# Performance work log

Measured on AMD Instinct MI355X. Metric: run time of the kernel, lower is better.

Reference implementation:

```python
import jax, jax.numpy as jnp
import numpy as np

B, HP, WP, EMB = 32, 56, 56, 256
HEADS, WX, WY = 8, 7, 7
WS = WX * WY

# relative position index table (constant int lookup, matches torch buffer)
_idx = np.indices((WX, WY)).transpose(1, 2, 0).reshape(WS, 2)
_REL = _idx[None, :, :] - _idx[:, None, :] + np.array([WX - 1, WY - 1])  # [49,49,2]

# shift masks (constants)
_m = WX * (WY // 2)
_row = np.zeros((WS, WS), np.float32)
_row[-_m:, :-_m] = -np.inf
_row[:-_m, -_m:] = -np.inf
# rearrange '(r w1) (c w2) -> (w1 r) (w2 c)' with w1=WX, w2=WY
_col = _row.reshape(WS // WX, WX, WS // WY, WY).transpose(1, 0, 3, 2).reshape(WS, WS)
ROW_MASK = jnp.asarray(_row)
COL_MASK = jnp.asarray(_col)


def setup_inputs() -> dict:
    key = jax.random.key(0)
    k1, k2, k3 = jax.random.split(key, 3)
    x = jax.random.normal(k1, (B, HP, WP, EMB), jnp.float32)
    w1 = jax.random.normal(k2, (EMB, 3 * EMB), jnp.float32) * 0.02
    b1 = jnp.zeros((3 * EMB,), jnp.float32)
    pos_emb = jax.random.normal(k3, (2 * WX - 1, 2 * WY - 1), jnp.float32)
    return {"x": x, "w1": w1, "b1": b1, "pos_emb": pos_emb}


def reference(x, w1, b1, pos_emb):
    Bn, H, W, E = x.shape
    e = E // HEADS
    hdim = float(E) / HEADS
    qkv = x @ w1 + b1                         # [B,H,W,3E]
    qkv = qkv.reshape(Bn, H, W, E, 3)         # (c k): c outer, k inner (interleaved QKV)
    # shifted: roll by (-WX)//2 = -4 for WX=7 (Python floor div, as in source)
    qkv = jnp.roll(qkv, ((-WX) // 2, (-WY) // 2), axis=(1, 2))
    Wh, Ww = H // WX, W // WY
    # split channel (e H): head index is INNER dim, as in source rearrange
    t = qkv.reshape(Bn, Wh, WX, Ww, WY, e, HEADS, 3)
    t = t.transpose(0, 6, 1, 3, 2, 4, 5, 7).reshape(Bn, HEADS, Wh, Ww, WS, e, 3)
    q, k, v = t[..., 0], t[..., 1], t[..., 2]
    attn = jnp.einsum('bhuvqe,bhuvke->bhuvqk', q, k) / jnp.sqrt(
        jnp.asarray(hdim, x.dtype))
    bias = pos_emb[_REL[:, :, 0], _REL[:, :, 1]]   # [49,49]
    attn = attn + bias
    # shift masks on last window row / last window column (corner gets both)
    attn = attn.at[:, :, -1, :, :, :].add(ROW_MASK)
    attn = attn.at[:, :, :, -1, :, :].add(COL_MASK)
    out = jnp.einsum('bhuvqk,bhuvke->bhuvqe', jax.nn.softmax(attn, axis=-1), v)
    # merge back: channel = e*HEADS + h
    out = out.reshape(Bn, HEADS, Wh, Ww, WX, WY, e)
    out = out.transpose(0, 2, 4, 3, 5, 6, 1).reshape(Bn, H, W, E)
    # reverse roll uses WX//2 = +3 (NOT the inverse of -4), faithful to source
    out = jnp.roll(out, (WX // 2, WY // 2), axis=(1, 2))
    return out
```

## Files before the change

kernel.cpp:

```cpp
#include <hip/hip_runtime.h>


typedef short bf16x8 __attribute__((ext_vector_type(8)));
typedef float f32x4 __attribute__((ext_vector_type(4)));
typedef unsigned short u16;
typedef u16 u16x8 __attribute__((ext_vector_type(8)));
typedef u16 u16x4 __attribute__((ext_vector_type(4)));

#define MFMA16(A, B, C) __builtin_amdgcn_mfma_f32_16x16x32_bf16((A), (B), (C), 0, 0, 0)

__device__ __forceinline__ u16 f2bf(float f) {
  union { float f; unsigned int u; } c; c.f = f;
  unsigned int uu = c.u;
  return (u16)((uu + 0x7fffu + ((uu >> 16) & 1u)) >> 16);
}

#define OFF_A   16384
#define OFF_POS 50176
#define SMEM_BYTES (50176 + 896)

__global__ void prep_w(const float* __restrict__ w1, const float* __restrict__ b1,
                       u16* __restrict__ wT, float* __restrict__ bp) {
  int g = blockIdx.x * 256 + threadIdx.x;
  float val = w1[g];
  int n = g % 768;
  int k = g / 768;
  int t = n % 3, c = n / 3;
  int np = (c & 7) * 96 + t * 32 + (c >> 3);
  wT[np * 256 + k] = f2bf(val);
  if (g < 768) {
    int t2 = g % 3, c2 = g / 3;
    bp[(c2 & 7) * 96 + t2 * 32 + (c2 >> 3)] = b1[g];
  }
}

__launch_bounds__(512, 4)
__global__ void swin_fused(const float* __restrict__ x, const u16* __restrict__ wT,
                           const float* __restrict__ bp, const float* __restrict__ pos,
                           float* __restrict__ out) {
  __shared__ __align__(16) char smem[SMEM_BYTES];
  const int tid  = threadIdx.x;
  const int wave = tid >> 6;
  const int lane = tid & 63;
  const int quad = lane >> 4;
  const int l16  = lane & 15;
  const int blk  = blockIdx.x;
  const int b = blk >> 6, u = (blk >> 3) & 7, v = blk & 7;

  float* sPos = (float*)(smem + OFF_POS);
  if (tid < 169) sPos[(tid / 13) * 16 + tid % 13] = pos[tid];

  {
    const int xbase = b * (56 * 56 * 256);
#pragma unroll
    for (int it = 0; it < 4; ++it) {
      int idx = tid + it * 512;
      int row = idx >> 5;
      int ck  = idx & 31;
      char* dst = smem + OFF_A + row * 512 + ((ck ^ (row & 7)) << 4);
      u16x8 val{};
      if (row < 49) {
        int i = row / 7, j = row % 7;
        int sh = u * 7 + i + 4; if (sh >= 56) sh -= 56;
        int sw = v * 7 + j + 4; if (sw >= 56) sw -= 56;
        const float4* src = (const float4*)(x + xbase + (sh * 56 + sw) * 256 + ck * 8);
        float4 f0 = src[0];
        float4 f1 = src[1];
        val.s0 = f2bf(f0.x); val.s1 = f2bf(f0.y); val.s2 = f2bf(f0.z); val.s3 = f2bf(f0.w);
        val.s4 = f2bf(f1.x); val.s5 = f2bf(f1.y); val.s6 = f2bf(f1.z); val.s7 = f2bf(f1.w);
      }
      *(u16x8*)dst = val;
    }
  }

  float bias[6];
#pragma unroll
  for (int i = 0; i < 6; ++i) bias[i] = bp[wave * 96 + i * 16 + l16];

  __syncthreads();

  const char* sA = smem + OFF_A;
  char* T = smem + wave * 2048;
  bf16x8 qf[4], kf[4], vf[2][2];

#pragma unroll
  for (int t = 0; t < 3; ++t) {
    f32x4 acc[4][2];
#pragma unroll
    for (int m = 0; m < 4; ++m) {
      acc[m][0] = (f32x4){0.f, 0.f, 0.f, 0.f};
      acc[m][1] = (f32x4){0.f, 0.f, 0.f, 0.f};
    }
    const u16* gB0 = wT + (wave * 96 + t * 32 + l16) * 256 + quad * 8;
    const u16* gB1 = gB0 + 16 * 256;
    bf16x8 b0 = *(const bf16x8*)gB0;
    bf16x8 b1 = *(const bf16x8*)gB1;
#pragma unroll
    for (int ks = 0; ks < 8; ++ks) {
      bf16x8 b0n, b1n;
      if (ks < 7) {
        b0n = *(const bf16x8*)(gB0 + (ks + 1) * 32);
        b1n = *(const bf16x8*)(gB1 + (ks + 1) * 32);
      }
#pragma unroll
      for (int m = 0; m < 4; ++m) {
        int row = m * 16 + l16;
        bf16x8 am = *(const bf16x8*)(sA + row * 512 + (((ks * 4 + quad) ^ (row & 7)) << 4));
        acc[m][0] = MFMA16(am, b0, acc[m][0]);
        acc[m][1] = MFMA16(am, b1, acc[m][1]);
      }
      if (ks < 7) { b0 = b0n; b1 = b1n; }
    }

    if (t < 2) {
#pragma unroll
      for (int hm = 0; hm < 2; ++hm) {
#pragma unroll
        for (int m2 = 0; m2 < 2; ++m2) {
          int m = hm * 2 + m2;
#pragma unroll
          for (int r = 0; r < 4; ++r) {
            int rb = m2 * 16 + quad * 4 + r;
            int sw = (rb >> 2) & 3;
            char* base = T + (rb ^ ((rb >> 2) & 1)) * 64;
            *(u16*)(base + ((((l16 >> 3) ^ sw) << 4) | ((l16 & 7) << 1)))
                = f2bf(acc[m][0][r] + bias[t * 2]);
            *(u16*)(base + (((((l16 >> 3) + 2) ^ sw) << 4) | ((l16 & 7) << 1)))
                = f2bf(acc[m][1][r] + bias[t * 2 + 1]);
          }
        }
        asm volatile("s_waitcnt lgkmcnt(0)" ::: "memory");
#pragma unroll
        for (int m2 = 0; m2 < 2; ++m2) {
          int m = hm * 2 + m2;
          int rb = m2 * 16 + l16;
          int sw = (rb >> 2) & 3;
          const bf16x8 fr2 = *(const bf16x8*)(T + (rb ^ ((rb >> 2) & 1)) * 64
                                                + ((quad ^ sw) << 4));
          if (t == 0) qf[m] = fr2; else kf[m] = fr2;
        }
        asm volatile("s_waitcnt lgkmcnt(0)" ::: "memory");
      }
    } else {
#pragma unroll
      for (int i = 0; i < 2; ++i) {
#pragma unroll
        for (int m = 0; m < 4; ++m) {
          int kc = m * 2 + (quad >> 1);
          int hb = (quad & 1) << 3;
          u16x4 w;
          w.x = f2bf(acc[m][i][0] + bias[4 + i]);
          w.y = f2bf(acc[m][i][1] + bias[4 + i]);
          w.z = f2bf(acc[m][i][2] + bias[4 + i]);
          w.w = f2bf(acc[m][i][3] + bias[4 + i]);
          *(u16x4*)(T + l16 * 128 + (((kc ^ (l16 & 7)) << 4) | hb)) = w;
        }
        asm volatile("s_waitcnt lgkmcnt(0)" ::: "memory");
#pragma unroll
        for (int ph = 0; ph < 2; ++ph)
          vf[ph][i] = *(const bf16x8*)(T + l16 * 128 + (((ph * 4 + quad) ^ (l16 & 7)) << 4));
        asm volatile("s_waitcnt lgkmcnt(0)" ::: "memory");
      }
    }
  }

  int ki[4], kj[4]; bool kok[4], kro[4], kco[4];
#pragma unroll
  for (int n = 0; n < 4; ++n) {
    int k = n * 16 + l16;
    ki[n] = k / 7; kj[n] = k % 7;
    kok[n] = (k < 49);
    kro[n] = (ki[n] >= 4);
    kco[n] = (kj[n] >= 4);
  }
  const bool rowm = (u == 7), colm = (v == 7);
  const float scale = 0.17677669529663687f;

  f32x4 o[4][2];
  {
    char* T2 = T;
#pragma unroll
    for (int m = 0; m < 4; ++m) {
      f32x4 s[4];
#pragma unroll
      for (int n = 0; n < 4; ++n)
        s[n] = MFMA16(qf[m], kf[n], ((f32x4){0.f, 0.f, 0.f, 0.f}));

      float inv[4];
#pragma unroll
      for (int r = 0; r < 4; ++r) {
        int q = m * 16 + quad * 4 + r;
        int qi = q / 7, qj = q % 7;
        bool qro = (qi >= 4), qco = (qj >= 4);
        int cm = 102 - qi * 16 - qj;
        float sum = 0.f;
#pragma unroll
        for (int n = 0; n < 4; ++n) {
          bool bad = (!kok[n]) || (rowm && (qro != kro[n])) || (colm && (qco != kco[n]));
          float sv = bad ? -1e30f
                         : fminf(s[n][r] * scale + sPos[ki[n] * 16 + kj[n] + cm], 30.f);
          float p = __expf(sv);
          s[n][r] = p;
          sum += p;
        }
        sum += __shfl_xor(sum, 1);
        sum += __shfl_xor(sum, 2);
        sum += __shfl_xor(sum, 4);
        sum += __shfl_xor(sum, 8);
        inv[r] = 1.f / sum;
      }

#pragma unroll
      for (int n = 0; n < 4; ++n)
#pragma unroll
        for (int r = 0; r < 4; ++r) {
          int row16 = quad * 4 + r;
          int ch = (2 * n + (l16 >> 3) + 2 * quad) & 7;
          *(u16*)(T2 + row16 * 128 + ((ch << 4) | ((l16 & 7) << 1))) = f2bf(s[n][r]);
        }
      asm volatile("s_waitcnt lgkmcnt(0)" ::: "memory");
      bf16x8 pa0 = *(const bf16x8*)(T2 + l16 * 128 + (((quad + 2 * (l16 >> 2)) & 7) << 4));
      bf16x8 pa1 = *(const bf16x8*)(T2 + l16 * 128 + (((4 + quad + 2 * (l16 >> 2)) & 7) << 4));
      asm volatile("s_waitcnt lgkmcnt(0)" ::: "memory");

      o[m][0] = MFMA16(pa0, vf[0][0], ((f32x4){0.f, 0.f, 0.f, 0.f}));
      o[m][0] = MFMA16(pa1, vf[1][0], o[m][0]);
      o[m][1] = MFMA16(pa0, vf[0][1], ((f32x4){0.f, 0.f, 0.f, 0.f}));
      o[m][1] = MFMA16(pa1, vf[1][1], o[m][1]);
#pragma unroll
      for (int i = 0; i < 2; ++i)
#pragma unroll
        for (int r = 0; r < 4; ++r) o[m][i][r] *= inv[r];
    }
  }

  __syncthreads();
  {
    float* oLds = (float*)smem;
    const int hh = wave;
#pragma unroll
    for (int m = 0; m < 4; ++m)
#pragma unroll
      for (int r = 0; r < 4; ++r) {
        int row = m * 16 + quad * 4 + r;
        if (row < 49) {
          int t4 = row >> 2;
          int fr = (t4 + (t4 >> 1)) & 7;
#pragma unroll
          for (int n = 0; n < 2; ++n) {
            int ci = n * 32 + l16 * 2 + (hh >> 2);
            int cs = ci ^ fr;
            oLds[row * 256 + cs * 4 + (hh & 3)] = o[m][n][r];
          }
        }
      }
  }
  __syncthreads();

  {
    const int obase = b * (56 * 56 * 256);
    for (int i2 = tid; i2 < 49 * 64; i2 += 512) {
      int row = i2 >> 6, ck = i2 & 63;
      int ii = row / 7, jj = row % 7;
      int dh = u * 7 + ii + 3; if (dh >= 56) dh -= 56;
      int dw = v * 7 + jj + 3; if (dw >= 56) dw -= 56;
      int t4 = row >> 2;
      int fr = (t4 + (t4 >> 1)) & 7;
      f32x4 val = *(const f32x4*)((const float*)smem + row * 256 + 4 * (ck ^ fr));
      *(f32x4*)(out + obase + (dh * 56 + dw) * 256 + ck * 4) = val;
    }
  }
}

extern "C" void kernel_launch(void* const* d_in, const int* in_sizes, int n_in,
                              void* d_out, int out_size, void* d_ws, size_t ws_size,
                              hipStream_t stream) {
  const float* x   = (const float*)d_in[0];
  const float* w1  = (const float*)d_in[1];
  const float* b1  = (const float*)d_in[2];
  const float* pos = (const float*)d_in[3];
  const size_t need = (size_t)768 * 256 * 2 + 768 * 4;
  if (ws_size < need) return;
  u16*   wT = (u16*)d_ws;
  float* bp = (float*)((char*)d_ws + 768 * 256 * 2);
  prep_w<<<768, 256, 0, stream>>>(w1, b1, wT, bp);
  swin_fused<<<2048, 512, 0, stream>>>(x, wT, bp, pos, (float*)d_out);
}
```

Measured before the change: 295.0 us.

## Compute transposed scores and pass P to PV MFMA via shuffles instead of LDS

The score MFMA swaps its operands so each lane holds one query row across keys. The row-sum reduction becomes two shuffles, and normalization moves before the bf16 pack. P is converted with v_cvt_pk_bf16_f32 and rearranged into the A-operand layout through cross-lane shuffles, replacing the LDS write/read round trip with its waitcnts. Key-side mask and position indices are precomputed as packed per-lane bitfields. Risks include more shuffle instructions and bf16 rounding of already-normalized probabilities.

```diff
diff --git a/kernel.cpp b/kernel.cpp
--- a/kernel.cpp
+++ b/kernel.cpp
@@ -13,6 +13,28 @@
   union { float f; unsigned int u; } c; c.f = f;
   unsigned int uu = c.u;
   return (u16)((uu + 0x7fffu + ((uu >> 16) & 1u)) >> 16);
+}
+
+__device__ __forceinline__ unsigned int cvtpk(float lo, float hi) {
+  unsigned int r;
+  asm("v_cvt_pk_bf16_f32 %0, %1, %2" : "=v"(r) : "v"(lo), "v"(hi));
+  return r;
+}
+
+__device__ __forceinline__ bf16x8 xchg(unsigned int p0a, unsigned int p1a,
+                                       unsigned int p0b, unsigned int p1b,
+                                       int quad, int l16) {
+  int lo = ((quad & 1) << 5) | l16;
+  int hi = lo + 16;
+  int a0 = __shfl((int)p0a, lo), b0 = __shfl((int)p0b, lo);
+  int a1 = __shfl((int)p1a, lo), b1 = __shfl((int)p1b, lo);
+  int a2 = __shfl((int)p0a, hi), b2 = __shfl((int)p0b, hi);
+  int a3 = __shfl((int)p1a, hi), b3 = __shfl((int)p1b, hi);
+  bool h = quad >= 2;
+  union { int u[4]; bf16x8 v; } r;
+  r.u[0] = h ? b0 : a0; r.u[1] = h ? b1 : a1;
+  r.u[2] = h ? b2 : a2; r.u[3] = h ? b3 : a3;
+  return r.v;
 }
 
 #define OFF_A   16384
@@ -164,74 +186,68 @@
     }
   }
 
-  int ki[4], kj[4]; bool kok[4], kro[4], kco[4];
+  unsigned int pb[4], fl[4];
 #pragma unroll
   for (int n = 0; n < 4; ++n) {
-    int k = n * 16 + l16;
-    ki[n] = k / 7; kj[n] = k % 7;
-    kok[n] = (k < 49);
-    kro[n] = (ki[n] >= 4);
-    kco[n] = (kj[n] >= 4);
+    pb[n] = 0; fl[n] = 0;
+#pragma unroll
+    for (int r = 0; r < 4; ++r) {
+      int k = n * 16 + quad * 4 + r;
+      int ki2 = k / 7, kj2 = k % 7;
+      bool kok = (k < 49);
+      pb[n] |= (unsigned int)(kok ? ki2 * 16 + kj2 : 0) << (8 * r);
+      fl[n] |= ((unsigned int)kok << r) | ((unsigned int)(ki2 >= 4) << (8 + r))
+             | ((unsigned int)(kj2 >= 4) << (16 + r));
+    }
   }
   const bool rowm = (u == 7), colm = (v == 7);
   const float scale = 0.17677669529663687f;
 
   f32x4 o[4][2];
-  {
-    char* T2 = T;
-#pragma unroll
-    for (int m = 0; m < 4; ++m) {
-      f32x4 s[4];
-#pragma unroll
-      for (int n = 0; n < 4; ++n)
-        s[n] = MFMA16(qf[m], kf[n], ((f32x4){0.f, 0.f, 0.f, 0.f}));
-
-      float inv[4];
+#pragma unroll
+  for (int m = 0; m < 4; ++m) {
+    f32x4 st[4];
+#pragma unroll
+    for (int n = 0; n < 4; ++n)
+      st[n] = MFMA16(kf[n], qf[m], ((f32x4){0.f, 0.f, 0.f, 0.f}));
+
+    const int q = m * 16 + l16;
+    const int qi = q / 7, qj = q % 7;
+    const int cm = 102 - qi * 16 - qj;
+    const bool qro = (qi >= 4), qco = (qj >= 4);
+
+    float sum = 0.f;
+#pragma unroll
+    for (int n = 0; n < 4; ++n)
 #pragma unroll
       for (int r = 0; r < 4; ++r) {
-        int q = m * 16 + quad * 4 + r;
-        int qi = q / 7, qj = q % 7;
-        bool qro = (qi >= 4), qco = (qj >= 4);
-        int cm = 102 - qi * 16 - qj;
-        float sum = 0.f;
-#pragma unroll
-        for (int n = 0; n < 4; ++n) {
-          bool bad = (!kok[n]) || (rowm && (qro != kro[n])) || (colm && (qco != kco[n]));
-          float sv = bad ? -1e30f
-                         : fminf(s[n][r] * scale + sPos[ki[n] * 16 + kj[n] + cm], 30.f);
-          float p = __expf(sv);
-          s[n][r] = p;
-          sum += p;
-        }
-        sum += __shfl_xor(sum, 1);
-        sum += __shfl_xor(sum, 2);
-        sum += __shfl_xor(sum, 4);
-        sum += __shfl_xor(sum, 8);
-        inv[r] = 1.f / sum;
-      }
-
-#pragma unroll
-      for (int n = 0; n < 4; ++n)
-#pragma unroll
-        for (int r = 0; r < 4; ++r) {
-          int row16 = quad * 4 + r;
-          int ch = (2 * n + (l16 >> 3) + 2 * quad) & 7;
-          *(u16*)(T2 + row16 * 128 + ((ch << 4) | ((l16 & 7) << 1))) = f2bf(s[n][r]);
-        }
-      asm volatile("s_waitcnt lgkmcnt(0)" ::: "memory");
-      bf16x8 pa0 = *(const bf16x8*)(T2 + l16 * 128 + (((quad + 2 * (l16 >> 2)) & 7) << 4));
-      bf16x8 pa1 = *(const bf16x8*)(T2 + l16 * 128 + (((4 + quad + 2 * (l16 >> 2)) & 7) << 4));
-      asm volatile("s_waitcnt lgkmcnt(0)" ::: "memory");
-
-      o[m][0] = MFMA16(pa0, vf[0][0], ((f32x4){0.f, 0.f, 0.f, 0.f}));
-      o[m][0] = MFMA16(pa1, vf[1][0], o[m][0]);
-      o[m][1] = MFMA16(pa0, vf[0][1], ((f32x4){0.f, 0.f, 0.f, 0.f}));
-      o[m][1] = MFMA16(pa1, vf[1][1], o[m][1]);
-#pragma unroll
-      for (int i = 0; i < 2; ++i)
-#pragma unroll
-        for (int r = 0; r < 4; ++r) o[m][i][r] *= inv[r];
-    }
+        bool kok = (fl[n] >> r) & 1;
+        bool kro = (fl[n] >> (8 + r)) & 1;
+        bool kco = (fl[n] >> (16 + r)) & 1;
+        bool bad = (!kok) || (rowm && (qro != kro)) || (colm && (qco != kco));
+        int pidx = (int)((pb[n] >> (8 * r)) & 255) + cm;
+        float sv = bad ? -1e30f : fminf(st[n][r] * scale + sPos[pidx], 30.f);
+        float p = __expf(sv);
+        st[n][r] = p;
+        sum += p;
+      }
+    sum += __shfl_xor(sum, 16);
+    sum += __shfl_xor(sum, 32);
+    float inv = 1.f / sum;
+
+    unsigned int pk0[4], pk1[4];
+#pragma unroll
+    for (int n = 0; n < 4; ++n) {
+      pk0[n] = cvtpk(st[n][0] * inv, st[n][1] * inv);
+      pk1[n] = cvtpk(st[n][2] * inv, st[n][3] * inv);
+    }
+    bf16x8 pa0 = xchg(pk0[0], pk1[0], pk0[1], pk1[1], quad, l16);
+    bf16x8 pa1 = xchg(pk0[2], pk1[2], pk0[3], pk1[3], quad, l16);
+
+    o[m][0] = MFMA16(pa0, vf[0][0], ((f32x4){0.f, 0.f, 0.f, 0.f}));
+    o[m][0] = MFMA16(pa1, vf[1][0], o[m][0]);
+    o[m][1] = MFMA16(pa0, vf[0][1], ((f32x4){0.f, 0.f, 0.f, 0.f}));
+    o[m][1] = MFMA16(pa1, vf[1][1], o[m][1]);
   }
 
   __syncthreads();
```

Result: faster. 283.1 us (-4.0%).
